# Performance work log

Measured on AMD Instinct MI355X. Metric: run time of the kernel, lower is better.

The kernel has to match this reference:

```python
import jax, jax.numpy as jnp
import numpy as np

B, S, D, H = 4, 2048, 1024, 16
HD = D // H  # head dim = 64


def setup_inputs() -> dict:
    key = jax.random.key(0)
    ks = jax.random.split(key, 11)
    std = 1.0 / np.sqrt(D)
    return {
        "query": jax.random.normal(ks[0], (B, S, D), jnp.float32),
        "key": jax.random.normal(ks[1], (B, S, D), jnp.float32),
        "value": jax.random.normal(ks[2], (B, S, D), jnp.float32),
        "Wq": jax.random.normal(ks[3], (D, D), jnp.float32) * std,
        "bq": jnp.zeros((D,), jnp.float32),
        "Wk": jax.random.normal(ks[4], (D, D), jnp.float32) * std,
        "bk": jnp.zeros((D,), jnp.float32),
        "Wv": jax.random.normal(ks[5], (D, D), jnp.float32) * std,
        "bv": jnp.zeros((D,), jnp.float32),
        "Wo": jax.random.normal(ks[6], (D, D), jnp.float32) * std,
        "bo": jnp.zeros((D,), jnp.float32),
    }


def reference(query, key, value, Wq, bq, Wk, bk, Wv, bv, Wo, bo):
    scale = jnp.sqrt(jnp.float32(D))  # NOTE: module scales by sqrt(hid_dim), not sqrt(head_dim)
    # nn.Linear: x @ W.T + b
    def split_heads(x):
        return x.reshape(B, -1, H, HD).transpose(0, 2, 1, 3)  # [B,H,S,HD]
    Q = split_heads(query @ Wq.T + bq)
    K = split_heads(key @ Wk.T + bk)
    V = split_heads(value @ Wv.T + bv)
    energy = jnp.einsum("bhqd,bhkd->bhqk", Q, K) / scale  # [B,H,S,S]
    attention = jax.nn.softmax(energy, axis=-1)  # dropout is identity in eval / p=0
    X = jnp.einsum("bhqk,bhkd->bhqd", attention, V)  # [B,H,S,HD]
    X = X.transpose(0, 2, 1, 3).reshape(B, -1, D)  # [B,S,D]
    return X @ Wo.T + bo
```

## Files before the change

kernel.cpp:

```cpp
#include <hip/hip_runtime.h>
#include <stdint.h>

#define DEVI __device__ __forceinline__

typedef __attribute__((ext_vector_type(8))) __bf16 bf16x8;
typedef __attribute__((ext_vector_type(4))) __bf16 bf16x4;
typedef __attribute__((ext_vector_type(4))) float f32x4;
typedef __attribute__((ext_vector_type(4))) unsigned short u16x4;
typedef __attribute__((ext_vector_type(4))) unsigned int u32x4;
typedef unsigned short u16;

constexpr int Bn = 4, Sn = 2048, Dn = 1024, Hn = 16;
constexpr int Mn = Bn * Sn;
constexpr float QSCALE = 1.4426950408889634f / 32.0f;
constexpr float SSHIFT = -16.0f;

DEVI u16 f2bf(float f) {
  uint32_t u = __builtin_bit_cast(uint32_t, f);
  u += 0x7fffu + ((u >> 16) & 1u);
  return (u16)(u >> 16);
}

typedef __attribute__((address_space(1))) void gvoid;
typedef __attribute__((address_space(3))) void lvoid;
DEVI void gload_lds16(const void* g, void* l) {
  __builtin_amdgcn_global_load_lds((gvoid*)(uintptr_t)g,
                                   (lvoid*)(uint32_t)(uintptr_t)l, 16, 0, 0);
}

DEVI f32x4 mfma16(bf16x8 a, bf16x8 b, f32x4 c) {
  return __builtin_amdgcn_mfma_f32_16x16x32_bf16(a, b, c, 0, 0, 0);
}

struct CastArgs {
  const float* src[7];
  u16* dst[7];
  int n[7];
};

__global__ __launch_bounds__(256) void cast_kernel(CastArgs a) {
  const int seg = blockIdx.y;
  const float* __restrict__ src = a.src[seg];
  u16* __restrict__ dst = a.dst[seg];
  const int n = a.n[seg];
  const int stride = gridDim.x * 256 * 4;
  for (int i = (blockIdx.x * 256 + threadIdx.x) * 4; i < n; i += stride) {
    const float4 v = *reinterpret_cast<const float4*>(src + i);
    u16x4 p;
    p[0] = f2bf(v.x); p[1] = f2bf(v.y); p[2] = f2bf(v.z); p[3] = f2bf(v.w);
    *reinterpret_cast<u16x4*>(dst + i) = p;
  }
}

#define GEMM_PRE(Aptr, Btptr)                                                 \
  const int tid = threadIdx.x, lane = tid & 63, w = tid >> 6;                 \
  const int wr = w >> 2, wc = w & 3;                                          \
  const int c = lane & 15, g = lane >> 4;                                     \
  const int arow = tid >> 3;                                                  \
  const int aus = (tid & 7) ^ (arow & 7);                                     \
  const u16* aSrc = (Aptr) + (size_t)(m0 + arow + 64 * (aus >> 2)) * 1024     \
                    + (aus & 3) * 8;                                          \
  const u16* bSrc0 = (Btptr) + (size_t)(n0 + arow + 128 * (aus >> 2)) * 1024  \
                     + (aus & 3) * 8;                                         \
  const u16* bSrc1 = bSrc0 + (size_t)64 * 1024;                               \
  const int ldsOff = w * 1024;                                                \
  const int aBr = c * 128 + (((wr * 4 + g) ^ (c & 7)) << 4);                  \
  const int bBr = (wc & 1) * 8192 + c * 128                                   \
                  + ((((wc >> 1) * 4 + g) ^ (c & 7)) << 4);

#define GSTAGE(BUF, KT_)                                                      \
  {                                                                           \
    gload_lds16(aSrc + (KT_), (char*)As[BUF] + ldsOff);                       \
    gload_lds16(bSrc0 + (KT_), (char*)Bs[BUF] + ldsOff);                      \
    gload_lds16(bSrc1 + (KT_), (char*)Bs[BUF] + 8192 + ldsOff);               \
  }

#define GTILE(BUF, SBUF, KT)                                                  \
  {                                                                           \
    asm volatile("s_waitcnt vmcnt(3)" ::: "memory");                          \
    __builtin_amdgcn_sched_barrier(0);                                        \
    __builtin_amdgcn_s_barrier();                                             \
    __builtin_amdgcn_sched_barrier(0);                                        \
    GSTAGE(SBUF, ((KT) + 64) & 1023);                                         \
    bf16x8 af[4], bfq[4];                                                     \
    _Pragma("unroll")                                                         \
    for (int i = 0; i < 4; ++i)                                               \
      af[i] = *(const bf16x8*)((const char*)As[BUF] + aBr + i * 2048);        \
    _Pragma("unroll")                                                         \
    for (int i = 0; i < 4; ++i)                                               \
      bfq[i] = *(const bf16x8*)((const char*)Bs[BUF] + bBr + i * 2048);       \
    __builtin_amdgcn_s_setprio(1);                                            \
    _Pragma("unroll")                                                         \
    for (int mi = 0; mi < 4; ++mi)                                            \
      _Pragma("unroll")                                                       \
      for (int ni = 0; ni < 4; ++ni)                                          \
        acc[mi][ni] = mfma16(af[mi], bfq[ni], acc[mi][ni]);                   \
    __builtin_amdgcn_s_setprio(0);                                            \
  }

#define GEMM_LOOP                                                             \
  GSTAGE(0, 0);                                                               \
  GSTAGE(1, 32);                                                              \
  for (int kt = 0; kt < 960; kt += 96) {                                      \
    GTILE(0, 2, kt);                                                          \
    GTILE(1, 0, kt + 32);                                                     \
    GTILE(2, 1, kt + 64);                                                     \
  }                                                                           \
  GTILE(0, 2, 960);                                                           \
  GTILE(1, 0, 992);

struct QKVArgs {
  const u16 *Aq, *Ak, *Av, *Wq, *Wk, *Wv;
  const float *bq, *bk, *bv;
  u16 *Qh, *Kh, *Vt;
};

__global__ __launch_bounds__(512, 4)
void qkv_gemm(QKVArgs a) {
  __shared__ __align__(16) u16 As[3][128 * 32];
  __shared__ __align__(16) u16 Bs[3][256 * 32];

  const int raw = blockIdx.x;
  const int swz = (raw & 7) * 96 + (raw >> 3);
  const int which = swz >> 8;
  const int bid = swz & 255;
  const u16* __restrict__ A  = which == 0 ? a.Aq : which == 1 ? a.Ak : a.Av;
  const u16* __restrict__ Bt = which == 0 ? a.Wq : which == 1 ? a.Wk : a.Wv;
  const float* __restrict__ bias = which == 0 ? a.bq : which == 1 ? a.bk : a.bv;

  const int mt = bid >> 2, nt = bid & 3;
  const int m0 = mt * 128, n0 = nt * 256;

  GEMM_PRE(A, Bt)
  f32x4 acc[4][4] = {};
  GEMM_LOOP

  #pragma unroll
  for (int mi = 0; mi < 4; ++mi) {
    #pragma unroll
    for (int ni = 0; ni < 4; ++ni) {
      const int n = n0 + wc * 64 + ni * 16 + c;
      const float bv = bias[n];
      const int mb = m0 + wr * 64 + mi * 16 + g * 4;
      const f32x4 v = acc[mi][ni];
      const int h = n >> 6, hd = n & 63;
      if (which == 2) {
        const int b = mb >> 11, s = mb & 2047;
        u16x4 pk;
        #pragma unroll
        for (int j = 0; j < 4; ++j) pk[j] = f2bf(v[j] + bv);
        *(u16x4*)(a.Vt + ((size_t)((b * Hn + h) * 64 + hd)) * Sn + s) = pk;
      } else {
        u16* dst = which == 0 ? a.Qh : a.Kh;
        const float sc = which == 0 ? QSCALE : 1.0f;
        #pragma unroll
        for (int j = 0; j < 4; ++j) {
          const int m = mb + j;
          const int b = m >> 11, s = m & 2047;
          dst[(((size_t)(b * Hn + h) * Sn + s) << 6) + hd] = f2bf((v[j] + bv) * sc);
        }
      }
    }
  }
}

__global__ __launch_bounds__(512, 4)
void gemm_out(const u16* __restrict__ A, const u16* __restrict__ Bt,
              const float* __restrict__ bias, float* __restrict__ out) {
  __shared__ __align__(16) u16 As[3][128 * 32];
  __shared__ __align__(16) u16 Bs[3][256 * 32];

  const int raw = blockIdx.x;
  const int swz = (raw & 7) * 32 + (raw >> 3);
  const int mt = swz >> 2, nt = swz & 3;
  const int m0 = mt * 128, n0 = nt * 256;

  GEMM_PRE(A, Bt)
  f32x4 acc[4][4] = {};
  GEMM_LOOP

  #pragma unroll
  for (int mi = 0; mi < 4; ++mi) {
    #pragma unroll
    for (int ni = 0; ni < 4; ++ni) {
      const int n = n0 + wc * 64 + ni * 16 + c;
      const float bv = bias[n];
      const int mb = m0 + wr * 64 + mi * 16 + g * 4;
      const f32x4 v = acc[mi][ni];
      #pragma unroll
      for (int j = 0; j < 4; ++j)
        out[(size_t)(mb + j) * Dn + n] = v[j] + bv;
    }
  }
}

#undef GEMM_LOOP
#undef GTILE
#undef GSTAGE
#undef GEMM_PRE

__global__ __launch_bounds__(512, 4)
void flash_attn(const u16* __restrict__ Q, const u16* __restrict__ K,
                const u16* __restrict__ Vt, u16* __restrict__ X) {
  __shared__ __align__(16) u16 Ks[3][4096];
  __shared__ __align__(16) u16 Vs[3][4096];

  const int tid = threadIdx.x, lane = tid & 63, w = tid >> 6;
  const int bid = blockIdx.x;
  const int bh = bid & 63, qt = bid >> 6;
  const int b = bh >> 4, h = bh & 15;
  const int q0 = qt * 128 + w * 16;
  const int c = lane & 15, g = lane >> 4;

  const u16* Qb = Q + (size_t)bh * Sn * 64;
  const u16* Kb = K + (size_t)bh * Sn * 64;
  const u16* Vb = Vt + (size_t)bh * 64 * Sn;

  const int srow = tid >> 3;
  const int scol = (((tid & 7) * 16) ^ ((srow & 7) << 4)) >> 1;
  const int srcK = srow * 64 + scol;
  const int srcV = srow * Sn + scol;
  const int ldsOff = w * 1024;
#define STAGE(BUF, KV_)                                                   \
  {                                                                       \
    gload_lds16(Kb + (size_t)(KV_) * 64 + srcK, (char*)Ks[BUF] + ldsOff); \
    gload_lds16(Vb + (KV_) + srcV, (char*)Vs[BUF] + ldsOff);              \
  }

  const int laneB0 = c * 128 + ((g * 16) ^ ((c & 7) << 4));
  const int laneB1 = c * 128 + ((64 + g * 16) ^ ((c & 7) << 4));

  bf16x8 qf[2];
  #pragma unroll
  for (int ks = 0; ks < 2; ++ks)
    qf[ks] = *(const bf16x8*)(Qb + (size_t)(q0 + c) * 64 + ks * 32 + g * 8);

  bf16x8 ONES;
  #pragma unroll
  for (int e = 0; e < 8; ++e) ONES[e] = (__bf16)1.0f;
  const f32x4 SINITv = {SSHIFT, SSHIFT, SSHIFT, SSHIFT};

  f32x4 o[4] = {};
  f32x4 lacc = {};
  f32x4 scA[4], scB[4];

#define QK_BLOCK(KB, SCT)                                                     \
  {                                                                           \
    bf16x8 kfr[4];                                                            \
    _Pragma("unroll")                                                         \
    for (int kf = 0; kf < 4; ++kf)                                            \
      kfr[kf] = *(const bf16x8*)((const char*)Ks[KB] + laneB0 + kf * 2048);   \
    __builtin_amdgcn_s_setprio(1);                                            \
    _Pragma("unroll")                                                         \
    for (int kf = 0; kf < 4; ++kf)                                            \
      SCT[kf] = mfma16(kfr[kf], qf[0], SINITv);                               \
    __builtin_amdgcn_s_setprio(0);                                            \
    _Pragma("unroll")                                                         \
    for (int kf = 0; kf < 4; ++kf)                                            \
      kfr[kf] = *(const bf16x8*)((const char*)Ks[KB] + laneB1 + kf * 2048);   \
    __builtin_amdgcn_s_setprio(1);                                            \
    _Pragma("unroll")                                                         \
    for (int kf = 0; kf < 4; ++kf)                                            \
      SCT[kf] = mfma16(kfr[kf], qf[1], SCT[kf]);                              \
    __builtin_amdgcn_s_setprio(0);                                            \
  }

#define FIN_BLOCK(VB, SCT)                                                    \
  {                                                                           \
    uint32_t wvv[4][2];                                                       \
    _Pragma("unroll")                                                         \
    for (int kf = 0; kf < 4; ++kf) {                                          \
      const float p0 = __builtin_exp2f(SCT[kf][0]);                           \
      const float p1 = __builtin_exp2f(SCT[kf][1]);                           \
      const float p2 = __builtin_exp2f(SCT[kf][2]);                           \
      const float p3 = __builtin_exp2f(SCT[kf][3]);                           \
      asm("v_cvt_pk_bf16_f32 %0, %1, %2" : "=v"(wvv[kf][0]) : "v"(p0), "v"(p1)); \
      asm("v_cvt_pk_bf16_f32 %0, %1, %2" : "=v"(wvv[kf][1]) : "v"(p2), "v"(p3)); \
    }                                                                         \
    bf16x8 pa[2];                                                             \
    _Pragma("unroll")                                                         \
    for (int ks2 = 0; ks2 < 2; ++ks2) {                                       \
      uint32_t ua = wvv[2 * ks2][0], ub = wvv[2 * ks2][1];                    \
      uint32_t uc = wvv[2 * ks2 + 1][0], ud = wvv[2 * ks2 + 1][1];            \
      asm("v_permlane32_swap_b32 %0, %1" : "+v"(ua), "+v"(uc));               \
      asm("v_permlane32_swap_b32 %0, %1" : "+v"(ub), "+v"(ud));               \
      asm("v_permlane16_swap_b32 %0, %1" : "+v"(ua), "+v"(uc));               \
      asm("v_permlane16_swap_b32 %0, %1" : "+v"(ub), "+v"(ud));               \
      const u32x4 uv = {ua, ub, uc, ud};                                      \
      pa[ks2] = __builtin_bit_cast(bf16x8, uv);                               \
    }                                                                         \
    lacc = mfma16(pa[0], ONES, lacc);                                         \
    lacc = mfma16(pa[1], ONES, lacc);                                         \
    {                                                                         \
      bf16x8 vfr[4];                                                          \
      _Pragma("unroll")                                                       \
      for (int nd = 0; nd < 4; ++nd)                                          \
        vfr[nd] = *(const bf16x8*)((const char*)Vs[VB] + laneB0 + nd * 2048); \
      __builtin_amdgcn_s_setprio(1);                                          \
      _Pragma("unroll")                                                       \
      for (int nd = 0; nd < 4; ++nd)                                          \
        o[nd] = mfma16(pa[0], vfr[nd], o[nd]);                                \
      __builtin_amdgcn_s_setprio(0);                                          \
      _Pragma("unroll")                                                       \
      for (int nd = 0; nd < 4; ++nd)                                          \
        vfr[nd] = *(const bf16x8*)((const char*)Vs[VB] + laneB1 + nd * 2048); \
      __builtin_amdgcn_s_setprio(1);                                          \
      _Pragma("unroll")                                                       \
      for (int nd = 0; nd < 4; ++nd)                                          \
        o[nd] = mfma16(pa[1], vfr[nd], o[nd]);                                \
      __builtin_amdgcn_s_setprio(0);                                          \
    }                                                                         \
  }

#define PIPE(KB, VB, SB, KV, CURT, NXTT)                                      \
  {                                                                           \
    asm volatile("s_waitcnt vmcnt(0)" ::: "memory");                          \
    __builtin_amdgcn_sched_barrier(0);                                        \
    __builtin_amdgcn_s_barrier();                                             \
    __builtin_amdgcn_sched_barrier(0);                                        \
    STAGE(SB, (KV) + 128);                                                    \
    QK_BLOCK(KB, NXTT);                                                       \
    FIN_BLOCK(VB, CURT);                                                      \
  }

  STAGE(0, 0);
  STAGE(1, 64);
  asm volatile("s_waitcnt vmcnt(2)" ::: "memory");
  __builtin_amdgcn_sched_barrier(0);
  __builtin_amdgcn_s_barrier();
  __builtin_amdgcn_sched_barrier(0);
  QK_BLOCK(0, scA);

  for (int kv = 0; kv < 1920; kv += 384) {
    PIPE(1, 0, 2, kv,       scA, scB);
    PIPE(2, 1, 0, kv + 64,  scB, scA);
    PIPE(0, 2, 1, kv + 128, scA, scB);
    PIPE(1, 0, 2, kv + 192, scB, scA);
    PIPE(2, 1, 0, kv + 256, scA, scB);
    PIPE(0, 2, 1, kv + 320, scB, scA);
  }
  asm volatile("s_waitcnt vmcnt(0)" ::: "memory");
  __builtin_amdgcn_sched_barrier(0);
  __builtin_amdgcn_s_barrier();
  __builtin_amdgcn_sched_barrier(0);
  QK_BLOCK(1, scB);
  FIN_BLOCK(0, scA);
  FIN_BLOCK(1, scB);
#undef PIPE
#undef FIN_BLOCK
#undef QK_BLOCK
#undef STAGE

  #pragma unroll
  for (int j = 0; j < 4; ++j) {
    const float rn = 1.0f / lacc[j];
    const int s = q0 + g * 4 + j;
    u16* dst = X + (size_t)(b * Sn + s) * Dn + h * 64 + c;
    #pragma unroll
    for (int nd = 0; nd < 4; ++nd)
      dst[nd * 16] = f2bf(o[nd][j] * rn);
  }
}

extern "C" void kernel_launch(void* const* d_in, const int* in_sizes, int n_in,
                              void* d_out, int out_size, void* d_ws, size_t ws_size,
                              hipStream_t stream) {
  (void)in_sizes; (void)n_in; (void)out_size; (void)ws_size;
  const float* query = (const float*)d_in[0];
  const float* key_  = (const float*)d_in[1];
  const float* value = (const float*)d_in[2];
  const float* Wq = (const float*)d_in[3];
  const float* bq = (const float*)d_in[4];
  const float* Wk = (const float*)d_in[5];
  const float* bk = (const float*)d_in[6];
  const float* Wv = (const float*)d_in[7];
  const float* bv = (const float*)d_in[8];
  const float* Wo = (const float*)d_in[9];
  const float* bo = (const float*)d_in[10];

  char* ws = (char*)d_ws;
  size_t off = 0;
  auto alloc = [&](size_t bytes) {
    void* p = ws + off;
    off += (bytes + 255) & ~(size_t)255;
    return p;
  };
  const size_t actB = (size_t)Mn * Dn * 2;
  const size_t wB = (size_t)Dn * Dn * 2;
  u16* qbuf = (u16*)alloc(actB);
  u16* kbuf = (u16*)alloc(actB);
  u16* vbuf = (u16*)alloc(actB);
  u16* wqb = (u16*)alloc(wB);
  u16* wkb = (u16*)alloc(wB);
  u16* wvb = (u16*)alloc(wB);
  u16* wob = (u16*)alloc(wB);
  u16* Qh = (u16*)alloc(actB);
  u16* Kh = (u16*)alloc(actB);
  u16* Vt = (u16*)alloc(actB);
  u16* Xb = qbuf;

  CastArgs ca;
  ca.src[0] = query; ca.src[1] = key_; ca.src[2] = value;
  ca.src[3] = Wq; ca.src[4] = Wk; ca.src[5] = Wv; ca.src[6] = Wo;
  ca.dst[0] = qbuf; ca.dst[1] = kbuf; ca.dst[2] = vbuf;
  ca.dst[3] = wqb; ca.dst[4] = wkb; ca.dst[5] = wvb; ca.dst[6] = wob;
  ca.n[0] = ca.n[1] = ca.n[2] = Mn * Dn;
  ca.n[3] = ca.n[4] = ca.n[5] = ca.n[6] = Dn * Dn;
  cast_kernel<<<dim3(1024, 7), 256, 0, stream>>>(ca);

  QKVArgs qa;
  qa.Aq = qbuf; qa.Ak = kbuf; qa.Av = vbuf;
  qa.Wq = wqb; qa.Wk = wkb; qa.Wv = wvb;
  qa.bq = bq; qa.bk = bk; qa.bv = bv;
  qa.Qh = Qh; qa.Kh = Kh; qa.Vt = Vt;
  qkv_gemm<<<dim3(768), 512, 0, stream>>>(qa);

  flash_attn<<<dim3(Bn * Hn * (Sn / 128)), 512, 0, stream>>>(Qh, Kh, Vt, Xb);
  gemm_out<<<dim3(256), 512, 0, stream>>>(Xb, wob, bo, (float*)d_out);
}
```

Measured before the change: 210.9 us.

## Fuse fp32-to-bf16 activation cast into QKV GEMM via fp32 LDS tiles

The QKV projection GEMM now streams fp32 query/key/value straight into LDS and converts to bf16 in registers with v_cvt_pk_bf16_f32 before the MFMAs. This drops the separate cast pass over the three large activation tensors and its bf16 write-and-reread round trip; the cast kernel now only converts the weights. To fit fp32 A tiles in LDS, the GEMM tile shrinks from 128x256 to 128x128 with twice as many blocks, which lowers per-block reuse of the weight tiles and adds conversion ALU work inside the inner loop.

```diff
diff --git a/kernel.cpp b/kernel.cpp
--- a/kernel.cpp
+++ b/kernel.cpp
@@ -33,9 +33,9 @@
 }
 
 struct CastArgs {
-  const float* src[7];
-  u16* dst[7];
-  int n[7];
+  const float* src[4];
+  u16* dst[4];
+  int n[4];
 };
 
 __global__ __launch_bounds__(256) void cast_kernel(CastArgs a) {
@@ -52,96 +52,103 @@
   }
 }
 
-#define GEMM_PRE(Aptr, Btptr)                                                 \
-  const int tid = threadIdx.x, lane = tid & 63, w = tid >> 6;                 \
-  const int wr = w >> 2, wc = w & 3;                                          \
-  const int c = lane & 15, g = lane >> 4;                                     \
-  const int arow = tid >> 3;                                                  \
-  const int aus = (tid & 7) ^ (arow & 7);                                     \
-  const u16* aSrc = (Aptr) + (size_t)(m0 + arow + 64 * (aus >> 2)) * 1024     \
-                    + (aus & 3) * 8;                                          \
-  const u16* bSrc0 = (Btptr) + (size_t)(n0 + arow + 128 * (aus >> 2)) * 1024  \
-                     + (aus & 3) * 8;                                         \
-  const u16* bSrc1 = bSrc0 + (size_t)64 * 1024;                               \
-  const int ldsOff = w * 1024;                                                \
-  const int aBr = c * 128 + (((wr * 4 + g) ^ (c & 7)) << 4);                  \
-  const int bBr = (wc & 1) * 8192 + c * 128                                   \
-                  + ((((wc >> 1) * 4 + g) ^ (c & 7)) << 4);
-
-#define GSTAGE(BUF, KT_)                                                      \
-  {                                                                           \
-    gload_lds16(aSrc + (KT_), (char*)As[BUF] + ldsOff);                       \
-    gload_lds16(bSrc0 + (KT_), (char*)Bs[BUF] + ldsOff);                      \
-    gload_lds16(bSrc1 + (KT_), (char*)Bs[BUF] + 8192 + ldsOff);               \
-  }
-
-#define GTILE(BUF, SBUF, KT)                                                  \
+struct QKVArgs {
+  const float *Aq, *Ak, *Av;
+  const u16 *Wq, *Wk, *Wv;
+  const float *bq, *bk, *bv;
+  u16 *Qh, *Kh, *Vt;
+};
+
+__global__ __launch_bounds__(512, 4)
+void qkv_gemm(QKVArgs a) {
+  __shared__ __align__(16) float Asf[3][128 * 32];
+  __shared__ __align__(16) u16 Bs[3][128 * 32];
+
+  const int raw = blockIdx.x;
+  const int swz = (raw & 7) * 192 + (raw >> 3);
+  const int which = swz >> 9;
+  const int bid = swz & 511;
+  const float* __restrict__ A = which == 0 ? a.Aq : which == 1 ? a.Ak : a.Av;
+  const u16* __restrict__ Bt  = which == 0 ? a.Wq : which == 1 ? a.Wk : a.Wv;
+  const float* __restrict__ bias = which == 0 ? a.bq : which == 1 ? a.bk : a.bv;
+
+  const int mt = bid >> 3, nt = bid & 7;
+  const int m0 = mt * 128, n0 = nt * 128;
+
+  const int tid = threadIdx.x, lane = tid & 63, w = tid >> 6;
+  const int wr = w >> 1, wc = w & 1;
+  const int c = lane & 15, g = lane >> 4;
+
+  const int arow = tid >> 3;
+  const int aus = (tid & 7) ^ (arow & 7);
+  const float* aSrc = A + (size_t)(m0 + arow) * 1024 + aus * 4;
+  const u16* bSrc = Bt + (size_t)(n0 + arow + 64 * (aus >> 2)) * 1024 + (aus & 3) * 8;
+  const int ldsOff = w * 1024;
+
+  const int aB0 = (wr * 32 + c) * 128 + (((g * 2) ^ (c & 7)) << 4);
+  const int bB0 = c * 128 + (((wc * 4 + g) ^ (c & 7)) << 4);
+
+  f32x4 acc[2][4] = {};
+
+#define QSTAGE(BUF, KT_)                                                      \
+  {                                                                           \
+    gload_lds16(aSrc + (KT_), (char*)Asf[BUF] + ldsOff);                      \
+    gload_lds16(aSrc + 65536 + (KT_), (char*)Asf[BUF] + 8192 + ldsOff);       \
+    gload_lds16(bSrc + (KT_), (char*)Bs[BUF] + ldsOff);                      \
+  }
+
+#define QTILE(BUF, SBUF, KT)                                                  \
   {                                                                           \
     asm volatile("s_waitcnt vmcnt(3)" ::: "memory");                          \
     __builtin_amdgcn_sched_barrier(0);                                        \
     __builtin_amdgcn_s_barrier();                                             \
     __builtin_amdgcn_sched_barrier(0);                                        \
-    GSTAGE(SBUF, ((KT) + 64) & 1023);                                         \
-    bf16x8 af[4], bfq[4];                                                     \
-    _Pragma("unroll")                                                         \
-    for (int i = 0; i < 4; ++i)                                               \
-      af[i] = *(const bf16x8*)((const char*)As[BUF] + aBr + i * 2048);        \
-    _Pragma("unroll")                                                         \
-    for (int i = 0; i < 4; ++i)                                               \
-      bfq[i] = *(const bf16x8*)((const char*)Bs[BUF] + bBr + i * 2048);       \
+    QSTAGE(SBUF, ((KT) + 64) & 1023);                                         \
+    bf16x8 bfq[4];                                                            \
+    _Pragma("unroll")                                                         \
+    for (int ni = 0; ni < 4; ++ni)                                            \
+      bfq[ni] = *(const bf16x8*)((const char*)Bs[BUF] + bB0 + ni * 2048);     \
+    bf16x8 af[2];                                                             \
+    _Pragma("unroll")                                                         \
+    for (int mi = 0; mi < 2; ++mi) {                                          \
+      const f32x4 alo = *(const f32x4*)((const char*)Asf[BUF] + (aB0 + mi * 2048));        \
+      const f32x4 ahi = *(const f32x4*)((const char*)Asf[BUF] + ((aB0 ^ 16) + mi * 2048)); \
+      uint32_t w0_, w1_, w2_, w3_;                                            \
+      asm("v_cvt_pk_bf16_f32 %0, %1, %2" : "=v"(w0_) : "v"(alo[0]), "v"(alo[1])); \
+      asm("v_cvt_pk_bf16_f32 %0, %1, %2" : "=v"(w1_) : "v"(alo[2]), "v"(alo[3])); \
+      asm("v_cvt_pk_bf16_f32 %0, %1, %2" : "=v"(w2_) : "v"(ahi[0]), "v"(ahi[1])); \
+      asm("v_cvt_pk_bf16_f32 %0, %1, %2" : "=v"(w3_) : "v"(ahi[2]), "v"(ahi[3])); \
+      const u32x4 uv_ = {w0_, w1_, w2_, w3_};                                 \
+      af[mi] = __builtin_bit_cast(bf16x8, uv_);                               \
+    }                                                                         \
     __builtin_amdgcn_s_setprio(1);                                            \
     _Pragma("unroll")                                                         \
-    for (int mi = 0; mi < 4; ++mi)                                            \
+    for (int mi = 0; mi < 2; ++mi)                                            \
       _Pragma("unroll")                                                       \
       for (int ni = 0; ni < 4; ++ni)                                          \
         acc[mi][ni] = mfma16(af[mi], bfq[ni], acc[mi][ni]);                   \
     __builtin_amdgcn_s_setprio(0);                                            \
   }
 
-#define GEMM_LOOP                                                             \
-  GSTAGE(0, 0);                                                               \
-  GSTAGE(1, 32);                                                              \
-  for (int kt = 0; kt < 960; kt += 96) {                                      \
-    GTILE(0, 2, kt);                                                          \
-    GTILE(1, 0, kt + 32);                                                     \
-    GTILE(2, 1, kt + 64);                                                     \
-  }                                                                           \
-  GTILE(0, 2, 960);                                                           \
-  GTILE(1, 0, 992);
-
-struct QKVArgs {
-  const u16 *Aq, *Ak, *Av, *Wq, *Wk, *Wv;
-  const float *bq, *bk, *bv;
-  u16 *Qh, *Kh, *Vt;
-};
-
-__global__ __launch_bounds__(512, 4)
-void qkv_gemm(QKVArgs a) {
-  __shared__ __align__(16) u16 As[3][128 * 32];
-  __shared__ __align__(16) u16 Bs[3][256 * 32];
-
-  const int raw = blockIdx.x;
-  const int swz = (raw & 7) * 96 + (raw >> 3);
-  const int which = swz >> 8;
-  const int bid = swz & 255;
-  const u16* __restrict__ A  = which == 0 ? a.Aq : which == 1 ? a.Ak : a.Av;
-  const u16* __restrict__ Bt = which == 0 ? a.Wq : which == 1 ? a.Wk : a.Wv;
-  const float* __restrict__ bias = which == 0 ? a.bq : which == 1 ? a.bk : a.bv;
-
-  const int mt = bid >> 2, nt = bid & 3;
-  const int m0 = mt * 128, n0 = nt * 256;
-
-  GEMM_PRE(A, Bt)
-  f32x4 acc[4][4] = {};
-  GEMM_LOOP
+  QSTAGE(0, 0);
+  QSTAGE(1, 32);
+  for (int kt = 0; kt < 960; kt += 96) {
+    QTILE(0, 2, kt);
+    QTILE(1, 0, kt + 32);
+    QTILE(2, 1, kt + 64);
+  }
+  QTILE(0, 2, 960);
+  QTILE(1, 0, 992);
+#undef QTILE
+#undef QSTAGE
 
   #pragma unroll
-  for (int mi = 0; mi < 4; ++mi) {
+  for (int mi = 0; mi < 2; ++mi) {
     #pragma unroll
     for (int ni = 0; ni < 4; ++ni) {
       const int n = n0 + wc * 64 + ni * 16 + c;
       const float bv = bias[n];
-      const int mb = m0 + wr * 64 + mi * 16 + g * 4;
+      const int mb = m0 + wr * 32 + mi * 16 + g * 4;
       const f32x4 v = acc[mi][ni];
       const int h = n >> 6, hd = n & 63;
       if (which == 2) {
@@ -175,9 +182,62 @@
   const int mt = swz >> 2, nt = swz & 3;
   const int m0 = mt * 128, n0 = nt * 256;
 
-  GEMM_PRE(A, Bt)
+  const int tid = threadIdx.x, lane = tid & 63, w = tid >> 6;
+  const int wr = w >> 2, wc = w & 3;
+  const int c = lane & 15, g = lane >> 4;
+  const int arow = tid >> 3;
+  const int aus = (tid & 7) ^ (arow & 7);
+  const u16* aSrc = A + (size_t)(m0 + arow + 64 * (aus >> 2)) * 1024 + (aus & 3) * 8;
+  const u16* bSrc0 = Bt + (size_t)(n0 + arow + 128 * (aus >> 2)) * 1024 + (aus & 3) * 8;
+  const u16* bSrc1 = bSrc0 + (size_t)64 * 1024;
+  const int ldsOff = w * 1024;
+  const int aBr = c * 128 + (((wr * 4 + g) ^ (c & 7)) << 4);
+  const int bBr = (wc & 1) * 8192 + c * 128
+                  + ((((wc >> 1) * 4 + g) ^ (c & 7)) << 4);
+
   f32x4 acc[4][4] = {};
-  GEMM_LOOP
+
+#define OSTAGE(BUF, KT_)                                                      \
+  {                                                                           \
+    gload_lds16(aSrc + (KT_), (char*)As[BUF] + ldsOff);                       \
+    gload_lds16(bSrc0 + (KT_), (char*)Bs[BUF] + ldsOff);                      \
+    gload_lds16(bSrc1 + (KT_), (char*)Bs[BUF] + 8192 + ldsOff);               \
+  }
+
+#define OTILE(BUF, SBUF, KT)                                                  \
+  {                                                                           \
+    asm volatile("s_waitcnt vmcnt(3)" ::: "memory");                          \
+    __builtin_amdgcn_sched_barrier(0);                                        \
+    __builtin_amdgcn_s_barrier();                                             \
+    __builtin_amdgcn_sched_barrier(0);                                        \
+    OSTAGE(SBUF, ((KT) + 64) & 1023);                                         \
+    bf16x8 af[4], bfq[4];                                                     \
+    _Pragma("unroll")                                                         \
+    for (int i = 0; i < 4; ++i)                                               \
+      af[i] = *(const bf16x8*)((const char*)As[BUF] + aBr + i * 2048);        \
+    _Pragma("unroll")                                                         \
+    for (int i = 0; i < 4; ++i)                                               \
+      bfq[i] = *(const bf16x8*)((const char*)Bs[BUF] + bBr + i * 2048);       \
+    __builtin_amdgcn_s_setprio(1);                                            \
+    _Pragma("unroll")                                                         \
+    for (int mi = 0; mi < 4; ++mi)                                            \
+      _Pragma("unroll")                                                       \
+      for (int ni = 0; ni < 4; ++ni)                                          \
+        acc[mi][ni] = mfma16(af[mi], bfq[ni], acc[mi][ni]);                   \
+    __builtin_amdgcn_s_setprio(0);                                            \
+  }
+
+  OSTAGE(0, 0);
+  OSTAGE(1, 32);
+  for (int kt = 0; kt < 960; kt += 96) {
+    OTILE(0, 2, kt);
+    OTILE(1, 0, kt + 32);
+    OTILE(2, 1, kt + 64);
+  }
+  OTILE(0, 2, 960);
+  OTILE(1, 0, 992);
+#undef OTILE
+#undef OSTAGE
 
   #pragma unroll
   for (int mi = 0; mi < 4; ++mi) {
@@ -193,11 +253,6 @@
     }
   }
 }
-
-#undef GEMM_LOOP
-#undef GTILE
-#undef GSTAGE
-#undef GEMM_PRE
 
 __global__ __launch_bounds__(512, 4)
 void flash_attn(const u16* __restrict__ Q, const u16* __restrict__ K,
@@ -387,9 +442,6 @@
   };
   const size_t actB = (size_t)Mn * Dn * 2;
   const size_t wB = (size_t)Dn * Dn * 2;
-  u16* qbuf = (u16*)alloc(actB);
-  u16* kbuf = (u16*)alloc(actB);
-  u16* vbuf = (u16*)alloc(actB);
   u16* wqb = (u16*)alloc(wB);
   u16* wkb = (u16*)alloc(wB);
   u16* wvb = (u16*)alloc(wB);
@@ -397,23 +449,20 @@
   u16* Qh = (u16*)alloc(actB);
   u16* Kh = (u16*)alloc(actB);
   u16* Vt = (u16*)alloc(actB);
-  u16* Xb = qbuf;
+  u16* Xb = (u16*)alloc(actB);
 
   CastArgs ca;
-  ca.src[0] = query; ca.src[1] = key_; ca.src[2] = value;
-  ca.src[3] = Wq; ca.src[4] = Wk; ca.src[5] = Wv; ca.src[6] = Wo;
-  ca.dst[0] = qbuf; ca.dst[1] = kbuf; ca.dst[2] = vbuf;
-  ca.dst[3] = wqb; ca.dst[4] = wkb; ca.dst[5] = wvb; ca.dst[6] = wob;
-  ca.n[0] = ca.n[1] = ca.n[2] = Mn * Dn;
-  ca.n[3] = ca.n[4] = ca.n[5] = ca.n[6] = Dn * Dn;
-  cast_kernel<<<dim3(1024, 7), 256, 0, stream>>>(ca);
+  ca.src[0] = Wq; ca.src[1] = Wk; ca.src[2] = Wv; ca.src[3] = Wo;
+  ca.dst[0] = wqb; ca.dst[1] = wkb; ca.dst[2] = wvb; ca.dst[3] = wob;
+  ca.n[0] = ca.n[1] = ca.n[2] = ca.n[3] = Dn * Dn;
+  cast_kernel<<<dim3(512, 4), 256, 0, stream>>>(ca);
 
   QKVArgs qa;
-  qa.Aq = qbuf; qa.Ak = kbuf; qa.Av = vbuf;
+  qa.Aq = query; qa.Ak = key_; qa.Av = value;
   qa.Wq = wqb; qa.Wk = wkb; qa.Wv = wvb;
   qa.bq = bq; qa.bk = bk; qa.bv = bv;
   qa.Qh = Qh; qa.Kh = Kh; qa.Vt = Vt;
-  qkv_gemm<<<dim3(768), 512, 0, stream>>>(qa);
+  qkv_gemm<<<dim3(1536), 512, 0, stream>>>(qa);
 
   flash_attn<<<dim3(Bn * Hn * (Sn / 128)), 512, 0, stream>>>(Qh, Kh, Vt, Xb);
   gemm_out<<<dim3(256), 512, 0, stream>>>(Xb, wob, bo, (float*)d_out);
```

New measurement: 206.5 us (median of 2 runs). 1.02x faster.
